# Kernel optimization log

Measured on AMD Instinct MI355X. Metric: run time of the kernel, lower is better.

## Reference

```python
import jax, jax.numpy as jnp
import numpy as np

B, N_PER, P_PER = 64, 64, 2016   # graphs, nodes/graph, pairs/graph (C(64,2))
IN_DIM, HID, OUT = 64, 128, 10
EDGE_P = 0.125


def _build_graph_structures():
    """Integer preprocessing replicating build_2sets_from_embeddings's
    combinatorics (pairs, iso_type source, triangle-based 2-set edges)."""
    rng = np.random.default_rng(0)
    n, b = N_PER, B
    A = rng.random((b, n, n)) < EDGE_P
    A = np.triu(A, 1)
    A = A | A.transpose(0, 2, 1)                      # symmetric, no self loops
    gs, us, vs = np.nonzero(A)                        # directed edges, both dirs
    edge_index = np.stack([gs * n + us, gs * n + vs]).astype(np.int64)
    batch = np.repeat(np.arange(b), n).astype(np.int64)
    iu, iv = np.triu_indices(n, 1)                    # local pair (u<v) lists
    pidx = np.full((n, n), -1, np.int64)
    pidx[iu, iv] = np.arange(P_PER)
    pidx[iv, iu] = np.arange(P_PER)                   # symmetric lookup = sorted()
    pair_u = (np.arange(b)[:, None] * n + iu[None, :]).ravel().astype(np.int64)
    pair_v = (np.arange(b)[:, None] * n + iv[None, :]).ravel().astype(np.int64)
    iso_type = A[:, iu, iv].astype(np.float32).ravel()[:, None]  # [B*P_PER,1]
    # 2-set edges: pair (u,v) -> sorted(v,w) and sorted(u,w) for every common
    # neighbor w of u and v (matches _build_2set_edges exactly)
    common = A[:, iu, :] & A[:, iv, :]                # (B, P_PER, n)
    g2, ps, ws = np.nonzero(common)
    u, v = iu[ps], iv[ps]
    d1 = pidx[v, ws]
    d2 = pidx[u, ws]
    src = np.concatenate([g2 * P_PER + ps, g2 * P_PER + ps])
    dst = np.concatenate([g2 * P_PER + d1, g2 * P_PER + d2])
    two_edges = np.stack([src, dst]).astype(np.int64)
    two_batch = np.repeat(np.arange(b), P_PER).astype(np.int64)
    return edge_index, batch, pair_u, pair_v, iso_type, two_edges, two_batch


def setup_inputs() -> dict:
    ei, batch, pu, pv, iso, te, tb = _build_graph_structures()
    key = jax.random.key(0)
    ks = jax.random.split(key, 16)
    w = lambda k, i, o: jax.random.normal(k, (i, o), jnp.float32) / np.float32(np.sqrt(i))
    two_in = 2 * HID + 1
    return {
        "x": jax.random.normal(ks[0], (B * N_PER, IN_DIM), jnp.float32),
        "g1_W1_0": w(ks[1], IN_DIM, HID), "g1_W2_0": w(ks[2], IN_DIM, HID),
        "g1_W1_1": w(ks[3], HID, HID),    "g1_W2_1": w(ks[4], HID, HID),
        "g1_W1_2": w(ks[5], HID, HID),    "g1_W2_2": w(ks[6], HID, HID),
        "k_W1_0": w(ks[7], two_in, HID),  "k_W2_0": w(ks[8], two_in, HID),
        "k_W1_1": w(ks[9], HID, HID),     "k_W2_1": w(ks[10], HID, HID),
        "c_W0": w(ks[11], 2 * HID, HID),  "c_b0": jnp.zeros((HID,), jnp.float32),
        "c_W1": w(ks[12], HID, OUT),      "c_b1": jnp.zeros((OUT,), jnp.float32),
        "iso_type": jnp.asarray(iso),
        "edge_index": jnp.asarray(ei), "batch": jnp.asarray(batch),
        "pair_u": jnp.asarray(pu), "pair_v": jnp.asarray(pv),
        "two_edges": jnp.asarray(te), "two_batch": jnp.asarray(tb),
    }


def _mp_layer(h, ei, W1, W2):
    # relu( h @ W1 + scatter_add_{dst}( h[src] @ W2 ) )  -- OneGNNLayer / KSetLayer
    msg = h[ei[0]] @ W2
    agg = jax.ops.segment_sum(msg, ei[1], num_segments=h.shape[0])
    return jax.nn.relu(h @ W1 + agg)


def reference(x, g1_W1_0, g1_W2_0, g1_W1_1, g1_W2_1, g1_W1_2, g1_W2_2,
              k_W1_0, k_W2_0, k_W1_1, k_W2_1,
              c_W0, c_b0, c_W1, c_b1,
              iso_type, edge_index, batch, pair_u, pair_v, two_edges, two_batch):
    h = _mp_layer(x, edge_index, g1_W1_0, g1_W2_0)
    h = _mp_layer(h, edge_index, g1_W1_1, g1_W2_1)
    h = _mp_layer(h, edge_index, g1_W1_2, g1_W2_2)
    graph_emb_1 = jax.ops.segment_sum(h, batch, num_segments=B)
    # 2-set features: [h_u, h_v, iso_type]  -> [P, 2H+1]
    two_x = jnp.concatenate([h[pair_u], h[pair_v], iso_type], axis=1)
    h2 = _mp_layer(two_x, two_edges, k_W1_0, k_W2_0)
    h2 = _mp_layer(h2, two_edges, k_W1_1, k_W2_1)
    graph_emb_2 = jax.ops.segment_sum(h2, two_batch, num_segments=B)
    combined = jnp.concatenate([graph_emb_1, graph_emb_2], axis=1)
    hc = jax.nn.relu(combined @ c_W0 + c_b0)   # Dropout(p=0.5) inactive in eval
    return hc @ c_W1 + c_b1
```

## Files before the change

kernel.cpp:

```cpp
#include <hip/hip_runtime.h>
#include <hip/hip_bf16.h>


typedef short s16x8 __attribute__((ext_vector_type(8)));
typedef float f32x4 __attribute__((ext_vector_type(4)));

__device__ __forceinline__ unsigned short f2bf(float f) {
  union { float f; unsigned u; } x; x.f = f;
  unsigned r = (x.u + 0x7fffu + ((x.u >> 16) & 1u)) >> 16;
  return (unsigned short)r;
}
__device__ __forceinline__ float bf2f(unsigned short h) {
  union { unsigned u; float f; } x; x.u = ((unsigned)h) << 16;
  return x.f;
}
__device__ __forceinline__ float4 ldbf4(const unsigned short* p) {
  ushort4 q = *(const ushort4*)p;
  return make_float4(bf2f(q.x), bf2f(q.y), bf2f(q.z), bf2f(q.w));
}
__device__ __forceinline__ void stbf4(unsigned short* p, float4 v) {
  ushort4 q;
  q.x = f2bf(v.x); q.y = f2bf(v.y); q.z = f2bf(v.z); q.w = f2bf(v.w);
  *(ushort4*)p = q;
}
__device__ __forceinline__ float4 ld4(const float* p) { return *(const float4*)p; }

template<int KCS, int ASTR>
__device__ __forceinline__ void mfma_dual_lds(
    const unsigned short* A, const unsigned short* Wfrag,
    f32x4 (&accA)[8], f32x4 (&accB)[8])
{
  const int lane = threadIdx.x & 63;
  const int wv = threadIdx.x >> 6;
  const int row = wv * 16 + (lane & 15);
  const int k0 = (lane >> 4) << 3;
  const unsigned short* ap = A + row * ASTR + k0;
  const unsigned short* wp = Wfrag + (size_t)lane * 8;
#pragma unroll
  for (int i = 0; i < 8; ++i) { accA[i] = (f32x4)0.f; accB[i] = (f32x4)0.f; }
#pragma unroll
  for (int kc = 0; kc < KCS; ++kc) {
    s16x8 af = *(const s16x8*)(ap + kc * 32);
#pragma unroll
    for (int nt = 0; nt < 8; ++nt) {
      s16x8 b0 = *(const s16x8*)(wp + ((size_t)((nt)*KCS + kc) << 9));
      s16x8 b1 = *(const s16x8*)(wp + ((size_t)((8 + nt) * KCS + kc) << 9));
      accA[nt] = __builtin_amdgcn_mfma_f32_16x16x32_bf16(af, b0, accA[nt], 0, 0, 0);
      accB[nt] = __builtin_amdgcn_mfma_f32_16x16x32_bf16(af, b1, accB[nt], 0, 0, 0);
    }
  }
}

template<int KCS, int ASTR>
__device__ __forceinline__ void mfma_dual_lds8(
    const unsigned short* A, const unsigned short* Wfrag,
    f32x4 (&accA)[4], f32x4 (&accB)[4])
{
  const int lane = threadIdx.x & 63;
  const int wv8 = threadIdx.x >> 6;
  const int rw = wv8 & 3, ch = wv8 >> 2;
  const int row = rw * 16 + (lane & 15);
  const int k0 = (lane >> 4) << 3;
  const unsigned short* ap = A + row * ASTR + k0;
  const unsigned short* wp = Wfrag + (size_t)lane * 8;
#pragma unroll
  for (int i = 0; i < 4; ++i) { accA[i] = (f32x4)0.f; accB[i] = (f32x4)0.f; }
  __builtin_amdgcn_s_setprio(1);
#pragma unroll
  for (int kc = 0; kc < KCS; ++kc) {
    s16x8 af = *(const s16x8*)(ap + kc * 32);
#pragma unroll
    for (int n4 = 0; n4 < 4; ++n4) {
      int nt = ch * 4 + n4;
      s16x8 b0 = *(const s16x8*)(wp + ((size_t)(nt * KCS + kc) << 9));
      s16x8 b1 = *(const s16x8*)(wp + ((size_t)((8 + nt) * KCS + kc) << 9));
      accA[n4] = __builtin_amdgcn_mfma_f32_16x16x32_bf16(af, b0, accA[n4], 0, 0, 0);
      accB[n4] = __builtin_amdgcn_mfma_f32_16x16x32_bf16(af, b1, accB[n4], 0, 0, 0);
    }
  }
  __builtin_amdgcn_s_setprio(0);
}

__device__ __forceinline__ void epi_lds8(const f32x4 (&accA)[4], const f32x4 (&accB)[4],
    unsigned short (*preS)[136], unsigned short (*msgS)[136])
{
  const int lane = threadIdx.x & 63;
  const int wv8 = threadIdx.x >> 6;
  const int rw = wv8 & 3, ch = wv8 >> 2;
  const int col = lane & 15;
  const int r0 = rw * 16 + ((lane >> 4) << 2);
  __syncthreads();
#pragma unroll
  for (int n4 = 0; n4 < 4; ++n4) {
    int nt = ch * 4 + n4;
#pragma unroll
    for (int r = 0; r < 4; ++r) {
      preS[r0 + r][nt * 16 + col] = f2bf(accA[n4][r]);
      msgS[r0 + r][nt * 16 + col] = f2bf(accB[n4][r]);
    }
  }
  __syncthreads();
}

__device__ __forceinline__ void epi_global(const f32x4 (&accA)[8], const f32x4 (&accB)[8],
    unsigned short (*sOut)[136], unsigned short* Ca, unsigned short* Cb, long tile)
{
  const int tid = threadIdx.x;
  const int lane = tid & 63;
  const int wv = tid >> 6;
  const int col = lane & 15;
  const int r0 = wv * 16 + ((lane >> 4) << 2);
  const long rowBase = tile * 64;
#pragma unroll
  for (int sel = 0; sel < 2; ++sel) {
    __syncthreads();
#pragma unroll
    for (int nt = 0; nt < 8; ++nt) {
#pragma unroll
      for (int r = 0; r < 4; ++r)
        sOut[r0 + r][nt * 16 + col] = f2bf(sel ? accB[nt][r] : accA[nt][r]);
    }
    __syncthreads();
    unsigned short* C = sel ? Cb : Ca;
#pragma unroll
    for (int i = 0; i < 4; ++i) {
      int fi = tid + i * 256;
      int row = fi >> 4;
      int c8 = fi & 15;
      *(uint4*)(C + (rowBase + row) * 128 + c8 * 8) = *(uint4*)&sOut[row][c8 * 8];
    }
  }
}

struct NArgs {
  const float* x;
  const int* ei;
  const int* gstart;
  const unsigned short *Wf0, *Wf1, *Wf2;
  unsigned short* Hn;
  float* ge1;
  int E1;
};

__global__ __launch_bounds__(512) void node_stage(NArgs a)
{
  __shared__ __align__(16) unsigned short hS[64][136];
  __shared__ __align__(16) unsigned short preS[64][136];
  __shared__ __align__(16) unsigned short msgS[64][136];
  __shared__ int ldeg[64], lcur[64], loff[65];
  __shared__ unsigned short ledge[1024];
  __shared__ float sge[128];

  const int b = blockIdx.x;
  const int t = threadIdx.x;
  const int base = b * 64;

  const int es = a.gstart[b], ee = a.gstart[b + 1];
  if (t < 64) ldeg[t] = 0;
  if (t < 128) sge[t] = 0.f;
  __syncthreads();
  for (int i = es + t; i < ee; i += 512)
    atomicAdd(&ldeg[a.ei[a.E1 + i] - base], 1);
  __syncthreads();
  if (t < 64) {
    int v = ldeg[t], s = v;
#pragma unroll
    for (int d = 1; d < 64; d <<= 1) {
      int o = __shfl_up(s, d, 64);
      if (t >= d) s += o;
    }
    loff[t] = s - v;
    lcur[t] = s - v;
    if (t == 63) loff[64] = s;
  }
  unsigned short* xs = &preS[0][0];
  for (int i = t; i < 64 * 64; i += 512) {
    int r = i >> 6, c = i & 63;
    xs[r * 72 + c] = f2bf(a.x[(size_t)(base + r) * 64 + c]);
  }
  __syncthreads();
  for (int i = es + t; i < ee; i += 512) {
    int s = a.ei[i] - base, d = a.ei[a.E1 + i] - base;
    int pos = atomicAdd(&lcur[d], 1);
    ledge[pos] = (unsigned short)s;
  }
  __syncthreads();

  f32x4 accA[4], accB[4];
  const int grp = t >> 5, f = (t & 31) * 4;

  mfma_dual_lds8<2, 72>(xs, a.Wf0, accA, accB);
  epi_lds8(accA, accB, preS, msgS);
  for (int r = grp; r < 64; r += 16) {
    float4 acc = ldbf4(&preS[r][f]);
    int j1 = loff[r + 1];
    for (int j = loff[r]; j < j1; ++j) {
      float4 m = ldbf4(&msgS[ledge[j]][f]);
      acc.x += m.x; acc.y += m.y; acc.z += m.z; acc.w += m.w;
    }
    stbf4(&hS[r][f], make_float4(fmaxf(acc.x, 0.f), fmaxf(acc.y, 0.f),
                                 fmaxf(acc.z, 0.f), fmaxf(acc.w, 0.f)));
  }
  __syncthreads();

  mfma_dual_lds8<4, 136>(&hS[0][0], a.Wf1, accA, accB);
  epi_lds8(accA, accB, preS, msgS);
  for (int r = grp; r < 64; r += 16) {
    float4 acc = ldbf4(&preS[r][f]);
    int j1 = loff[r + 1];
    for (int j = loff[r]; j < j1; ++j) {
      float4 m = ldbf4(&msgS[ledge[j]][f]);
      acc.x += m.x; acc.y += m.y; acc.z += m.z; acc.w += m.w;
    }
    stbf4(&hS[r][f], make_float4(fmaxf(acc.x, 0.f), fmaxf(acc.y, 0.f),
                                 fmaxf(acc.z, 0.f), fmaxf(acc.w, 0.f)));
  }
  __syncthreads();

  mfma_dual_lds8<4, 136>(&hS[0][0], a.Wf2, accA, accB);
  epi_lds8(accA, accB, preS, msgS);
  {
    float4 g = make_float4(0.f, 0.f, 0.f, 0.f);
    for (int r = grp; r < 64; r += 16) {
      float4 acc = ldbf4(&preS[r][f]);
      int j1 = loff[r + 1];
      for (int j = loff[r]; j < j1; ++j) {
        float4 m = ldbf4(&msgS[ledge[j]][f]);
        acc.x += m.x; acc.y += m.y; acc.z += m.z; acc.w += m.w;
      }
      float4 o = make_float4(fmaxf(acc.x, 0.f), fmaxf(acc.y, 0.f),
                             fmaxf(acc.z, 0.f), fmaxf(acc.w, 0.f));
      stbf4(&hS[r][f], o);
      g.x += o.x; g.y += o.y; g.z += o.z; g.w += o.w;
    }
    atomicAdd(&sge[f + 0], g.x);
    atomicAdd(&sge[f + 1], g.y);
    atomicAdd(&sge[f + 2], g.z);
    atomicAdd(&sge[f + 3], g.w);
  }
  __syncthreads();
  if (t < 128) a.ge1[b * 128 + t] = sge[t];
  for (int i = t; i < 1024; i += 512) {
    int row = i >> 4, c8 = i & 15;
    *(uint4*)(a.Hn + (size_t)(base + row) * 128 + c8 * 8) = *(uint4*)&hS[row][c8 * 8];
  }
}

__global__ __launch_bounds__(256) void hv_gemm(
    const unsigned short* __restrict__ Hn,
    const unsigned short* __restrict__ Wf3, const unsigned short* __restrict__ Wf4,
    unsigned short* __restrict__ HU1, unsigned short* __restrict__ HU2,
    unsigned short* __restrict__ HV1, unsigned short* __restrict__ HV2)
{
  __shared__ __align__(16) unsigned short hS[64][136];
  const int g = blockIdx.x >> 1;
  const int sel = blockIdx.x & 1;
  const int tid = threadIdx.x;
  const unsigned short* src = Hn + (size_t)g * 64 * 128;
#pragma unroll
  for (int i = 0; i < 4; ++i) {
    int fi = tid + i * 256;
    int row = fi >> 4, c8 = fi & 15;
    *(uint4*)&hS[row][c8 * 8] = *(const uint4*)(src + row * 128 + c8 * 8);
  }
  __syncthreads();
  f32x4 accA[8], accB[8];
  mfma_dual_lds<4, 136>(&hS[0][0], sel ? Wf4 : Wf3, accA, accB);
  epi_global(accA, accB, hS, sel ? HV1 : HU1, sel ? HV2 : HU2, g);
}

struct PrepArgs {
  const float* wa[6];
  const float* wb[6];
  unsigned short* Wf[6];
  float* ge2;
  const int* te; int E2;
  int* degP;
  const int* ei; int E1;
  int* gstart;
  int nCnt;
};

__global__ void prep(PrepArgs p)
{
  int bb = blockIdx.x, t = threadIdx.x;
  if (bb < 88) {
    int gid = bb * 256 + t;
    if (gid < 22528) {
      int pi, local, kcs, kclog;
      if (gid < 2048) { pi = 0; local = gid; kcs = 2; kclog = 1; }
      else { int r = gid - 2048; pi = 1 + (r >> 12); local = r & 4095; kcs = 4; kclog = 2; }
      int lane = local & 63;
      int t1 = local >> 6;
      int kc = t1 & (kcs - 1);
      int t2 = t1 >> kclog;
      int nt = t2 & 7;
      int wsel = t2 >> 3;
      const float* W = wsel ? p.wb[pi] : p.wa[pi];
      int k0 = kc * 32 + ((lane >> 4) << 3);
      int n = nt * 16 + (lane & 15);
      unsigned short tmp[8];
#pragma unroll
      for (int j = 0; j < 8; ++j) tmp[j] = f2bf(W[(size_t)(k0 + j) * 128 + n]);
      *(uint4*)(p.Wf[pi] + (size_t)local * 8) = *(uint4*)tmp;
    }
  } else if (bb < 120) {
    int i = (bb - 88) * 256 + t;
    if (i < 8192) p.ge2[i] = 0.f;
  } else if (bb < 120 + p.nCnt) {
    int e = (bb - 120) * 256 + t;
    if (e < p.E2) atomicAdd(&p.degP[p.te[p.E2 + e]], 1);
  } else {
    int e = (bb - 120 - p.nCnt) * 256 + t;
    if (e <= p.E1) {
      int ge = (e < p.E1) ? (p.ei[e] >> 6) : 64;
      int gp = (e > 0) ? (p.ei[e - 1] >> 6) : -1;
      for (int g = gp + 1; g <= ge; ++g) p.gstart[g] = e;
    }
  }
}

__global__ __launch_bounds__(256) void scan_reduce(const int* __restrict__ deg,
                                                   int* __restrict__ bsum, int n)
{
  __shared__ int s[256];
  int b = blockIdx.x, t = threadIdx.x;
  int base = b * 1024;
  int v = 0;
#pragma unroll
  for (int i = 0; i < 4; ++i) {
    int idx = base + t + i * 256;
    if (idx < n) v += deg[idx];
  }
  s[t] = v;
  __syncthreads();
  for (int d = 128; d > 0; d >>= 1) {
    if (t < d) s[t] += s[t + d];
    __syncthreads();
  }
  if (t == 0) bsum[b] = s[0];
}

__global__ __launch_bounds__(1024) void scan_partials(int* __restrict__ bsum, int nb)
{
  __shared__ int s[1024];
  int t = threadIdx.x;
  s[t] = (t < nb) ? bsum[t] : 0;
  __syncthreads();
  for (int d = 1; d < 1024; d <<= 1) {
    int v = (t >= d) ? s[t - d] : 0;
    __syncthreads();
    s[t] += v;
    __syncthreads();
  }
  if (t < nb) bsum[t] = (t == 0) ? 0 : s[t - 1];
  if (t == 1023) bsum[nb] = s[1023];
}

__global__ __launch_bounds__(256) void scan_final(const int* __restrict__ deg,
                                                  const int* __restrict__ bsum,
                                                  int* __restrict__ off,
                                                  int* __restrict__ cur, int n, int nb)
{
  __shared__ int s[256];
  int b = blockIdx.x, t = threadIdx.x;
  int base = b * 1024 + t * 4;
  int v0 = 0, v1 = 0, v2 = 0, v3 = 0;
  if (base + 0 < n) v0 = deg[base + 0];
  if (base + 1 < n) v1 = deg[base + 1];
  if (base + 2 < n) v2 = deg[base + 2];
  if (base + 3 < n) v3 = deg[base + 3];
  s[t] = v0 + v1 + v2 + v3;
  __syncthreads();
  for (int d = 1; d < 256; d <<= 1) {
    int v = (t >= d) ? s[t - d] : 0;
    __syncthreads();
    s[t] += v;
    __syncthreads();
  }
  int run = bsum[b] + ((t == 0) ? 0 : s[t - 1]);
  if (base + 0 < n) { off[base + 0] = run; cur[base + 0] = run; run += v0; }
  if (base + 1 < n) { off[base + 1] = run; cur[base + 1] = run; run += v1; }
  if (base + 2 < n) { off[base + 2] = run; cur[base + 2] = run; run += v2; }
  if (base + 3 < n) { off[base + 3] = run; cur[base + 3] = run; run += v3; }
  if (b == 0 && t == 0) off[n] = bsum[nb];
}

__global__ void csr_fill_pair(const int* __restrict__ te, int E2,
                              const int* __restrict__ pu, const int* __restrict__ pv,
                              const float* __restrict__ iso,
                              int* __restrict__ curP, int4* __restrict__ recP)
{
  int e = blockIdx.x * 256 + threadIdx.x;
  if (e >= E2) return;
  int s = te[e], d = te[E2 + e];
  int pos = atomicAdd(&curP[d], 1);
  recP[pos] = make_int4(pu[s], pv[s], __float_as_int(iso[s]), s);
}

__global__ __launch_bounds__(256) void gather_two0_t(
    const unsigned short* __restrict__ HU1, const unsigned short* __restrict__ HV1,
    const unsigned short* __restrict__ HU2, const unsigned short* __restrict__ HV2,
    const float* __restrict__ iso,
    const float* __restrict__ w1iso, const float* __restrict__ w2iso,
    const int* __restrict__ pu, const int* __restrict__ pv,
    const int* __restrict__ off, const int4* __restrict__ rec,
    unsigned short* __restrict__ out)
{
  __shared__ int offS[65];
  __shared__ int puS[64], pvS[64];
  __shared__ float isoS[64];
  __shared__ __align__(16) int4 recS[512];

  const int tid = threadIdx.x;
  int tile = (int)blockIdx.x;
  const int nT = (int)gridDim.x;
  if ((nT & 7) == 0)
    tile = (tile & 7) * (nT >> 3) + (tile >> 3);
  const int p0 = tile * 64;

  if (tid < 65) offS[tid] = off[p0 + tid];
  if (tid < 64) { puS[tid] = pu[p0 + tid]; pvS[tid] = pv[p0 + tid]; isoS[tid] = iso[p0 + tid]; }
  __syncthreads();
  const int e0 = offS[0];
  const int ecnt = offS[64] - e0;
  const bool useS = (ecnt <= 512);
  if (useS)
    for (int j = tid; j < ecnt; j += 256) recS[j] = rec[e0 + j];
  __syncthreads();

  const int grp = tid >> 5;
  const int f = (tid & 31) * 4;
  const float4 wi1 = ld4(w1iso + f);
  const float4 wi2 = ld4(w2iso + f);
  for (int pi = grp; pi < 64; pi += 8) {
    float4 a = ldbf4(HU1 + (size_t)puS[pi] * 128 + f);
    float4 b = ldbf4(HV1 + (size_t)pvS[pi] * 128 + f);
    float is0 = isoS[pi];
    float4 acc;
    acc.x = a.x + b.x + is0 * wi1.x;
    acc.y = a.y + b.y + is0 * wi1.y;
    acc.z = a.z + b.z + is0 * wi1.z;
    acc.w = a.w + b.w + is0 * wi1.w;
    int j = offS[pi], e1 = offS[pi + 1];
    for (; j + 1 < e1; j += 2) {
      int4 r0 = useS ? recS[j - e0] : rec[j];
      int4 r1 = useS ? recS[j + 1 - e0] : rec[j + 1];
      float4 mu0 = ldbf4(HU2 + (size_t)r0.x * 128 + f);
      float4 mv0 = ldbf4(HV2 + (size_t)r0.y * 128 + f);
      float4 mu1 = ldbf4(HU2 + (size_t)r1.x * 128 + f);
      float4 mv1 = ldbf4(HV2 + (size_t)r1.y * 128 + f);
      float i0 = __int_as_float(r0.z), i1 = __int_as_float(r1.z);
      acc.x += mu0.x + mv0.x + i0 * wi2.x + mu1.x + mv1.x + i1 * wi2.x;
      acc.y += mu0.y + mv0.y + i0 * wi2.y + mu1.y + mv1.y + i1 * wi2.y;
      acc.z += mu0.z + mv0.z + i0 * wi2.z + mu1.z + mv1.z + i1 * wi2.z;
      acc.w += mu0.w + mv0.w + i0 * wi2.w + mu1.w + mv1.w + i1 * wi2.w;
    }
    if (j < e1) {
      int4 r0 = useS ? recS[j - e0] : rec[j];
      float4 mu0 = ldbf4(HU2 + (size_t)r0.x * 128 + f);
      float4 mv0 = ldbf4(HV2 + (size_t)r0.y * 128 + f);
      float i0 = __int_as_float(r0.z);
      acc.x += mu0.x + mv0.x + i0 * wi2.x;
      acc.y += mu0.y + mv0.y + i0 * wi2.y;
      acc.z += mu0.z + mv0.z + i0 * wi2.z;
      acc.w += mu0.w + mv0.w + i0 * wi2.w;
    }
    stbf4(out + (size_t)(p0 + pi) * 128 + f,
          make_float4(fmaxf(acc.x, 0.f), fmaxf(acc.y, 0.f),
                      fmaxf(acc.z, 0.f), fmaxf(acc.w, 0.f)));
  }
}

__global__ __launch_bounds__(256) void pair_l1_fused(
    const unsigned short* __restrict__ H2,
    const unsigned short* __restrict__ Wfrag,
    const int* __restrict__ off, const int4* __restrict__ rec,
    float* __restrict__ ge2, int ppg)
{
  __shared__ __align__(16) unsigned short aggS[64][136];
  __shared__ int offS[65];
  __shared__ int recwS[768];
  __shared__ float sge[2][128];

  const int tid = threadIdx.x;
  int tile = (int)blockIdx.x;
  const int nT = (int)gridDim.x;
  if ((nT & 7) == 0)
    tile = (tile & 7) * (nT >> 3) + (tile >> 3);
  const int r0 = tile * 64;

  if (tid < 65) offS[tid] = off[r0 + tid];
  if (tid < 128) { sge[0][tid] = 0.f; sge[1][tid] = 0.f; }

  const int lane = tid & 63;
  const int wv = tid >> 6;
  const int arow = wv * 16 + (lane & 15);
  const int k0 = (lane >> 4) << 3;
  const unsigned short* hrow = H2 + (size_t)(r0 + arow) * 128 + k0;
  s16x8 ah[4];
#pragma unroll
  for (int kc = 0; kc < 4; ++kc) ah[kc] = *(const s16x8*)(hrow + kc * 32);

  __syncthreads();
  const int e0 = offS[0];
  const int ecnt = offS[64] - e0;
  const bool useS = (ecnt <= 768);
  if (useS)
    for (int j = tid; j < ecnt; j += 256) recwS[j] = rec[e0 + j].w;
  __syncthreads();

  {
    const int grp = tid >> 5, f = (tid & 31) * 4;
    for (int i = grp; i < 64; i += 8) {
      float4 acc = make_float4(0.f, 0.f, 0.f, 0.f);
      int j = offS[i], e1 = offS[i + 1];
      for (; j + 1 < e1; j += 2) {
        int s0 = useS ? recwS[j - e0] : rec[j].w;
        int s1 = useS ? recwS[j + 1 - e0] : rec[j + 1].w;
        float4 m0 = ldbf4(H2 + (size_t)s0 * 128 + f);
        float4 m1 = ldbf4(H2 + (size_t)s1 * 128 + f);
        acc.x += m0.x + m1.x; acc.y += m0.y + m1.y;
        acc.z += m0.z + m1.z; acc.w += m0.w + m1.w;
      }
      if (j < e1) {
        int s0 = useS ? recwS[j - e0] : rec[j].w;
        float4 m0 = ldbf4(H2 + (size_t)s0 * 128 + f);
        acc.x += m0.x; acc.y += m0.y; acc.z += m0.z; acc.w += m0.w;
      }
      stbf4(&aggS[i][f], acc);
    }
  }
  __syncthreads();

  const unsigned short* gp = &aggS[0][0] + arow * 136 + k0;
  const unsigned short* wp = Wfrag + (size_t)lane * 8;
  f32x4 acc[8];
#pragma unroll
  for (int nt = 0; nt < 8; ++nt) acc[nt] = (f32x4)0.f;
  __builtin_amdgcn_s_setprio(1);
#pragma unroll
  for (int kc = 0; kc < 4; ++kc) {
    s16x8 ag = *(const s16x8*)(gp + kc * 32);
#pragma unroll
    for (int nt = 0; nt < 8; ++nt) {
      s16x8 b0 = *(const s16x8*)(wp + ((size_t)(nt * 4 + kc) << 9));
      s16x8 b1 = *(const s16x8*)(wp + ((size_t)((8 + nt) * 4 + kc) << 9));
      acc[nt] = __builtin_amdgcn_mfma_f32_16x16x32_bf16(ah[kc], b0, acc[nt], 0, 0, 0);
      acc[nt] = __builtin_amdgcn_mfma_f32_16x16x32_bf16(ag, b1, acc[nt], 0, 0, 0);
    }
  }
  __builtin_amdgcn_s_setprio(0);

  const int half = wv >> 1;
  const int col0 = lane & 15;
#pragma unroll
  for (int nt = 0; nt < 8; ++nt) {
    float s = fmaxf(acc[nt][0], 0.f) + fmaxf(acc[nt][1], 0.f)
            + fmaxf(acc[nt][2], 0.f) + fmaxf(acc[nt][3], 0.f);
    atomicAdd(&sge[half][nt * 16 + col0], s);
  }
  __syncthreads();
  const int gLo = r0 / ppg;
  const int gHi = (r0 + 32) / ppg;
  if (tid < 128) atomicAdd(&ge2[gLo * 128 + tid], sge[0][tid]);
  else           atomicAdd(&ge2[gHi * 128 + (tid - 128)], sge[1][tid - 128]);
}

__global__ void classifier(const float* __restrict__ ge1, const float* __restrict__ ge2,
                           const float* __restrict__ W0, const float* __restrict__ b0,
                           const float* __restrict__ W1, const float* __restrict__ b1,
                           float* __restrict__ out)
{
  __shared__ float comb[256];
  __shared__ float hc[128];
  int g = blockIdx.x, t = threadIdx.x;
  comb[t]       = ge1[g * 128 + t];
  comb[t + 128] = ge2[g * 128 + t];
  __syncthreads();
  float s = b0[t];
  for (int k = 0; k < 256; ++k) s += comb[k] * W0[k * 128 + t];
  hc[t] = fmaxf(s, 0.f);
  __syncthreads();
  if (t < 10) {
    float s2 = b1[t];
    for (int k = 0; k < 128; ++k) s2 += hc[k] * W1[k * 10 + t];
    out[g * 10 + t] = s2;
  }
}

extern "C" void kernel_launch(void* const* d_in, const int* in_sizes, int n_in,
                              void* d_out, int out_size, void* d_ws, size_t ws_size,
                              hipStream_t stream)
{
  (void)n_in; (void)out_size; (void)ws_size;
  const float* x       = (const float*)d_in[0];
  const float* g1_W1_0 = (const float*)d_in[1];
  const float* g1_W2_0 = (const float*)d_in[2];
  const float* g1_W1_1 = (const float*)d_in[3];
  const float* g1_W2_1 = (const float*)d_in[4];
  const float* g1_W1_2 = (const float*)d_in[5];
  const float* g1_W2_2 = (const float*)d_in[6];
  const float* k_W1_0  = (const float*)d_in[7];
  const float* k_W2_0  = (const float*)d_in[8];
  const float* k_W1_1  = (const float*)d_in[9];
  const float* k_W2_1  = (const float*)d_in[10];
  const float* c_W0    = (const float*)d_in[11];
  const float* c_b0    = (const float*)d_in[12];
  const float* c_W1    = (const float*)d_in[13];
  const float* c_b1    = (const float*)d_in[14];
  const float* iso     = (const float*)d_in[15];
  const int*   ei      = (const int*)d_in[16];
  const int*   pu      = (const int*)d_in[18];
  const int*   pv      = (const int*)d_in[19];
  const int*   te      = (const int*)d_in[20];

  const int N  = in_sizes[0] / 64;
  const int E1 = in_sizes[16] / 2;
  const int P  = in_sizes[18];
  const int E2 = in_sizes[20] / 2;
  const int B  = 64;
  const int ppg = P / B;

  const size_t NH = (size_t)N * 128;
  const size_t PH = (size_t)P * 128;

  float* ge1 = (float*)d_ws;
  float* ge2 = ge1 + 8192;
  unsigned short* HU1 = (unsigned short*)(ge2 + 8192);
  unsigned short* HV1 = HU1 + NH;
  unsigned short* HU2 = HV1 + NH;
  unsigned short* HV2 = HU2 + NH;
  unsigned short* H2   = HV2 + NH;
  unsigned short* Hn   = H2 + PH;
  unsigned short* Wf0  = Hn + NH;
  unsigned short* Wf1  = Wf0 + 16384;
  unsigned short* Wf2  = Wf1 + 32768;
  unsigned short* Wf3  = Wf2 + 32768;
  unsigned short* Wf4  = Wf3 + 32768;
  unsigned short* Wf5  = Wf4 + 32768;

  size_t ipOff = ((size_t)((char*)(Wf5 + 32768) - (char*)d_ws) + 15) & ~(size_t)15;
  int4* recP   = (int4*)((char*)d_ws + ipOff);
  int* degP    = (int*)(recP + E2);
  int* offP    = degP + P;
  int* curP    = offP + P + 1;
  int* bsumP   = curP + P;
  int* gstartN = bsumP + 128;

  const int nbP  = (P + 1023) / 1024;
  const int nCnt = (E2 + 255) / 256;
  const int nBnd = (E1 + 256) / 256;

  hipMemsetAsync(degP, 0, (size_t)P * 4, stream);

  PrepArgs pa;
  pa.wa[0] = g1_W1_0;           pa.wb[0] = g1_W2_0;
  pa.wa[1] = g1_W1_1;           pa.wb[1] = g1_W2_1;
  pa.wa[2] = g1_W1_2;           pa.wb[2] = g1_W2_2;
  pa.wa[3] = k_W1_0;            pa.wb[3] = k_W2_0;
  pa.wa[4] = k_W1_0 + 128*128;  pa.wb[4] = k_W2_0 + 128*128;
  pa.wa[5] = k_W1_1;            pa.wb[5] = k_W2_1;
  pa.Wf[0] = Wf0; pa.Wf[1] = Wf1; pa.Wf[2] = Wf2;
  pa.Wf[3] = Wf3; pa.Wf[4] = Wf4; pa.Wf[5] = Wf5;
  pa.ge2 = ge2; pa.te = te; pa.E2 = E2; pa.degP = degP;
  pa.ei = ei; pa.E1 = E1; pa.gstart = gstartN; pa.nCnt = nCnt;
  prep<<<120 + nCnt + nBnd, 256, 0, stream>>>(pa);

  scan_reduce<<<nbP, 256, 0, stream>>>(degP, bsumP, P);
  scan_partials<<<1, 1024, 0, stream>>>(bsumP, nbP);
  scan_final<<<nbP, 256, 0, stream>>>(degP, bsumP, offP, curP, P, nbP);
  csr_fill_pair<<<nCnt, 256, 0, stream>>>(te, E2, pu, pv, iso, curP, recP);

  NArgs na;
  na.x = x; na.ei = ei; na.gstart = gstartN; na.E1 = E1;
  na.Wf0 = Wf0; na.Wf1 = Wf1; na.Wf2 = Wf2;
  na.Hn = Hn; na.ge1 = ge1;
  node_stage<<<B, 512, 0, stream>>>(na);

  hv_gemm<<<2 * B, 256, 0, stream>>>(Hn, Wf3, Wf4, HU1, HU2, HV1, HV2);

  gather_two0_t<<<P / 64, 256, 0, stream>>>(HU1, HV1, HU2, HV2, iso,
                                            k_W1_0 + 256 * 128, k_W2_0 + 256 * 128,
                                            pu, pv, offP, recP, H2);

  pair_l1_fused<<<P / 64, 256, 0, stream>>>(H2, Wf5, offP, recP, ge2, ppg);

  classifier<<<B, 128, 0, stream>>>(ge1, ge2, c_W0, c_b0, c_W1, c_b1, (float*)d_out);
}
```

Baseline: 304.7 us.

## Switch pair aggregation to edge-parallel LDS atomics and widen node stage to 1024 threads

```diff
diff --git a/kernel.cpp b/kernel.cpp
--- a/kernel.cpp
+++ b/kernel.cpp
@@ -52,51 +52,51 @@
 }
 
 template<int KCS, int ASTR>
-__device__ __forceinline__ void mfma_dual_lds8(
+__device__ __forceinline__ void mfma_dual_lds16(
     const unsigned short* A, const unsigned short* Wfrag,
-    f32x4 (&accA)[4], f32x4 (&accB)[4])
+    f32x4 (&accA)[2], f32x4 (&accB)[2])
 {
   const int lane = threadIdx.x & 63;
-  const int wv8 = threadIdx.x >> 6;
-  const int rw = wv8 & 3, ch = wv8 >> 2;
+  const int w16 = threadIdx.x >> 6;
+  const int rw = w16 & 3, ch = w16 >> 2;
   const int row = rw * 16 + (lane & 15);
   const int k0 = (lane >> 4) << 3;
   const unsigned short* ap = A + row * ASTR + k0;
   const unsigned short* wp = Wfrag + (size_t)lane * 8;
-#pragma unroll
-  for (int i = 0; i < 4; ++i) { accA[i] = (f32x4)0.f; accB[i] = (f32x4)0.f; }
+  accA[0] = (f32x4)0.f; accA[1] = (f32x4)0.f;
+  accB[0] = (f32x4)0.f; accB[1] = (f32x4)0.f;
   __builtin_amdgcn_s_setprio(1);
 #pragma unroll
   for (int kc = 0; kc < KCS; ++kc) {
     s16x8 af = *(const s16x8*)(ap + kc * 32);
 #pragma unroll
-    for (int n4 = 0; n4 < 4; ++n4) {
-      int nt = ch * 4 + n4;
+    for (int n2 = 0; n2 < 2; ++n2) {
+      int nt = ch * 2 + n2;
       s16x8 b0 = *(const s16x8*)(wp + ((size_t)(nt * KCS + kc) << 9));
       s16x8 b1 = *(const s16x8*)(wp + ((size_t)((8 + nt) * KCS + kc) << 9));
-      accA[n4] = __builtin_amdgcn_mfma_f32_16x16x32_bf16(af, b0, accA[n4], 0, 0, 0);
-      accB[n4] = __builtin_amdgcn_mfma_f32_16x16x32_bf16(af, b1, accB[n4], 0, 0, 0);
+      accA[n2] = __builtin_amdgcn_mfma_f32_16x16x32_bf16(af, b0, accA[n2], 0, 0, 0);
+      accB[n2] = __builtin_amdgcn_mfma_f32_16x16x32_bf16(af, b1, accB[n2], 0, 0, 0);
     }
   }
   __builtin_amdgcn_s_setprio(0);
 }
 
-__device__ __forceinline__ void epi_lds8(const f32x4 (&accA)[4], const f32x4 (&accB)[4],
+__device__ __forceinline__ void epi_lds16(const f32x4 (&accA)[2], const f32x4 (&accB)[2],
     unsigned short (*preS)[136], unsigned short (*msgS)[136])
 {
   const int lane = threadIdx.x & 63;
-  const int wv8 = threadIdx.x >> 6;
-  const int rw = wv8 & 3, ch = wv8 >> 2;
+  const int w16 = threadIdx.x >> 6;
+  const int rw = w16 & 3, ch = w16 >> 2;
   const int col = lane & 15;
   const int r0 = rw * 16 + ((lane >> 4) << 2);
   __syncthreads();
 #pragma unroll
-  for (int n4 = 0; n4 < 4; ++n4) {
-    int nt = ch * 4 + n4;
+  for (int n2 = 0; n2 < 2; ++n2) {
+    int nt = ch * 2 + n2;
 #pragma unroll
     for (int r = 0; r < 4; ++r) {
-      preS[r0 + r][nt * 16 + col] = f2bf(accA[n4][r]);
-      msgS[r0 + r][nt * 16 + col] = f2bf(accB[n4][r]);
+      preS[r0 + r][nt * 16 + col] = f2bf(accA[n2][r]);
+      msgS[r0 + r][nt * 16 + col] = f2bf(accB[n2][r]);
     }
   }
   __syncthreads();
@@ -142,7 +142,7 @@
   int E1;
 };
 
-__global__ __launch_bounds__(512) void node_stage(NArgs a)
+__global__ __launch_bounds__(1024) void node_stage(NArgs a)
 {
   __shared__ __align__(16) unsigned short hS[64][136];
   __shared__ __align__(16) unsigned short preS[64][136];
@@ -159,7 +159,7 @@
   if (t < 64) ldeg[t] = 0;
   if (t < 128) sge[t] = 0.f;
   __syncthreads();
-  for (int i = es + t; i < ee; i += 512)
+  for (int i = es + t; i < ee; i += 1024)
     atomicAdd(&ldeg[a.ei[a.E1 + i] - base], 1);
   __syncthreads();
   if (t < 64) {
@@ -174,24 +174,24 @@
     if (t == 63) loff[64] = s;
   }
   unsigned short* xs = &preS[0][0];
-  for (int i = t; i < 64 * 64; i += 512) {
+  for (int i = t; i < 64 * 64; i += 1024) {
     int r = i >> 6, c = i & 63;
     xs[r * 72 + c] = f2bf(a.x[(size_t)(base + r) * 64 + c]);
   }
   __syncthreads();
-  for (int i = es + t; i < ee; i += 512) {
+  for (int i = es + t; i < ee; i += 1024) {
     int s = a.ei[i] - base, d = a.ei[a.E1 + i] - base;
     int pos = atomicAdd(&lcur[d], 1);
     ledge[pos] = (unsigned short)s;
   }
   __syncthreads();
 
-  f32x4 accA[4], accB[4];
+  f32x4 accA[2], accB[2];
   const int grp = t >> 5, f = (t & 31) * 4;
 
-  mfma_dual_lds8<2, 72>(xs, a.Wf0, accA, accB);
-  epi_lds8(accA, accB, preS, msgS);
-  for (int r = grp; r < 64; r += 16) {
+  mfma_dual_lds16<2, 72>(xs, a.Wf0, accA, accB);
+  epi_lds16(accA, accB, preS, msgS);
+  for (int r = grp; r < 64; r += 32) {
     float4 acc = ldbf4(&preS[r][f]);
     int j1 = loff[r + 1];
     for (int j = loff[r]; j < j1; ++j) {
@@ -203,9 +203,9 @@
   }
   __syncthreads();
 
-  mfma_dual_lds8<4, 136>(&hS[0][0], a.Wf1, accA, accB);
-  epi_lds8(accA, accB, preS, msgS);
-  for (int r = grp; r < 64; r += 16) {
+  mfma_dual_lds16<4, 136>(&hS[0][0], a.Wf1, accA, accB);
+  epi_lds16(accA, accB, preS, msgS);
+  for (int r = grp; r < 64; r += 32) {
     float4 acc = ldbf4(&preS[r][f]);
     int j1 = loff[r + 1];
     for (int j = loff[r]; j < j1; ++j) {
@@ -217,11 +217,11 @@
   }
   __syncthreads();
 
-  mfma_dual_lds8<4, 136>(&hS[0][0], a.Wf2, accA, accB);
-  epi_lds8(accA, accB, preS, msgS);
+  mfma_dual_lds16<4, 136>(&hS[0][0], a.Wf2, accA, accB);
+  epi_lds16(accA, accB, preS, msgS);
   {
     float4 g = make_float4(0.f, 0.f, 0.f, 0.f);
-    for (int r = grp; r < 64; r += 16) {
+    for (int r = grp; r < 64; r += 32) {
       float4 acc = ldbf4(&preS[r][f]);
       int j1 = loff[r + 1];
       for (int j = loff[r]; j < j1; ++j) {
@@ -240,8 +240,8 @@
   }
   __syncthreads();
   if (t < 128) a.ge1[b * 128 + t] = sge[t];
-  for (int i = t; i < 1024; i += 512) {
-    int row = i >> 4, c8 = i & 15;
+  {
+    int row = t >> 4, c8 = t & 15;
     *(uint4*)(a.Hn + (size_t)(base + row) * 128 + c8 * 8) = *(uint4*)&hS[row][c8 * 8];
   }
 }
@@ -398,7 +398,7 @@
   recP[pos] = make_int4(pu[s], pv[s], __float_as_int(iso[s]), s);
 }
 
-__global__ __launch_bounds__(256) void gather_two0_t(
+__global__ __launch_bounds__(256) void gather_two0_ep(
     const unsigned short* __restrict__ HU1, const unsigned short* __restrict__ HV1,
     const unsigned short* __restrict__ HU2, const unsigned short* __restrict__ HV2,
     const float* __restrict__ iso,
@@ -407,10 +407,12 @@
     const int* __restrict__ off, const int4* __restrict__ rec,
     unsigned short* __restrict__ out)
 {
+  __shared__ float aggF[64][132];
   __shared__ int offS[65];
   __shared__ int puS[64], pvS[64];
   __shared__ float isoS[64];
   __shared__ __align__(16) int4 recS[512];
+  __shared__ unsigned short dstS[512];
 
   const int tid = threadIdx.x;
   int tile = (int)blockIdx.x;
@@ -421,66 +423,72 @@
 
   if (tid < 65) offS[tid] = off[p0 + tid];
   if (tid < 64) { puS[tid] = pu[p0 + tid]; pvS[tid] = pv[p0 + tid]; isoS[tid] = iso[p0 + tid]; }
+  {
+    float4 z = make_float4(0.f, 0.f, 0.f, 0.f);
+    float4* af = (float4*)&aggF[0][0];
+    for (int i = tid; i < 64 * 132 / 4; i += 256) af[i] = z;
+  }
   __syncthreads();
   const int e0 = offS[0];
   const int ecnt = offS[64] - e0;
   const bool useS = (ecnt <= 512);
-  if (useS)
+  if (useS) {
     for (int j = tid; j < ecnt; j += 256) recS[j] = rec[e0 + j];
+    if (tid < 64) {
+      int j1 = offS[tid + 1] - e0;
+      for (int j = offS[tid] - e0; j < j1; ++j) dstS[j] = (unsigned short)tid;
+    }
+  }
   __syncthreads();
 
   const int grp = tid >> 5;
   const int f = (tid & 31) * 4;
+  const float4 wi2 = ld4(w2iso + f);
+  for (int j = grp; j < ecnt; j += 8) {
+    int4 r; int d;
+    if (useS) { r = recS[j]; d = dstS[j]; }
+    else {
+      r = rec[e0 + j];
+      int lo = 0, hi = 64;
+      while (hi - lo > 1) { int mid = (lo + hi) >> 1; if (offS[mid] <= e0 + j) lo = mid; else hi = mid; }
+      d = lo;
+    }
+    float4 mu = ldbf4(HU2 + (size_t)r.x * 128 + f);
+    float4 mv = ldbf4(HV2 + (size_t)r.y * 128 + f);
+    float i0 = __int_as_float(r.z);
+    atomicAdd(&aggF[d][f + 0], mu.x + mv.x + i0 * wi2.x);
+    atomicAdd(&aggF[d][f + 1], mu.y + mv.y + i0 * wi2.y);
+    atomicAdd(&aggF[d][f + 2], mu.z + mv.z + i0 * wi2.z);
+    atomicAdd(&aggF[d][f + 3], mu.w + mv.w + i0 * wi2.w);
+  }
+  __syncthreads();
+
   const float4 wi1 = ld4(w1iso + f);
-  const float4 wi2 = ld4(w2iso + f);
   for (int pi = grp; pi < 64; pi += 8) {
     float4 a = ldbf4(HU1 + (size_t)puS[pi] * 128 + f);
     float4 b = ldbf4(HV1 + (size_t)pvS[pi] * 128 + f);
     float is0 = isoS[pi];
     float4 acc;
-    acc.x = a.x + b.x + is0 * wi1.x;
-    acc.y = a.y + b.y + is0 * wi1.y;
-    acc.z = a.z + b.z + is0 * wi1.z;
-    acc.w = a.w + b.w + is0 * wi1.w;
-    int j = offS[pi], e1 = offS[pi + 1];
-    for (; j + 1 < e1; j += 2) {
-      int4 r0 = useS ? recS[j - e0] : rec[j];
-      int4 r1 = useS ? recS[j + 1 - e0] : rec[j + 1];
-      float4 mu0 = ldbf4(HU2 + (size_t)r0.x * 128 + f);
-      float4 mv0 = ldbf4(HV2 + (size_t)r0.y * 128 + f);
-      float4 mu1 = ldbf4(HU2 + (size_t)r1.x * 128 + f);
-      float4 mv1 = ldbf4(HV2 + (size_t)r1.y * 128 + f);
-      float i0 = __int_as_float(r0.z), i1 = __int_as_float(r1.z);
-      acc.x += mu0.x + mv0.x + i0 * wi2.x + mu1.x + mv1.x + i1 * wi2.x;
-      acc.y += mu0.y + mv0.y + i0 * wi2.y + mu1.y + mv1.y + i1 * wi2.y;
-      acc.z += mu0.z + mv0.z + i0 * wi2.z + mu1.z + mv1.z + i1 * wi2.z;
-      acc.w += mu0.w + mv0.w + i0 * wi2.w + mu1.w + mv1.w + i1 * wi2.w;
-    }
-    if (j < e1) {
-      int4 r0 = useS ? recS[j - e0] : rec[j];
-      float4 mu0 = ldbf4(HU2 + (size_t)r0.x * 128 + f);
-      float4 mv0 = ldbf4(HV2 + (size_t)r0.y * 128 + f);
-      float i0 = __int_as_float(r0.z);
-      acc.x += mu0.x + mv0.x + i0 * wi2.x;
-      acc.y += mu0.y + mv0.y + i0 * wi2.y;
-      acc.z += mu0.z + mv0.z + i0 * wi2.z;
-      acc.w += mu0.w + mv0.w + i0 * wi2.w;
-    }
+    acc.x = a.x + b.x + is0 * wi1.x + aggF[pi][f + 0];
+    acc.y = a.y + b.y + is0 * wi1.y + aggF[pi][f + 1];
+    acc.z = a.z + b.z + is0 * wi1.z + aggF[pi][f + 2];
+    acc.w = a.w + b.w + is0 * wi1.w + aggF[pi][f + 3];
     stbf4(out + (size_t)(p0 + pi) * 128 + f,
           make_float4(fmaxf(acc.x, 0.f), fmaxf(acc.y, 0.f),
                       fmaxf(acc.z, 0.f), fmaxf(acc.w, 0.f)));
   }
 }
 
-__global__ __launch_bounds__(256) void pair_l1_fused(
+__global__ __launch_bounds__(256) void pair_l1_ep(
     const unsigned short* __restrict__ H2,
     const unsigned short* __restrict__ Wfrag,
     const int* __restrict__ off, const int4* __restrict__ rec,
     float* __restrict__ ge2, int ppg)
 {
-  __shared__ __align__(16) unsigned short aggS[64][136];
+  __shared__ float aggF[64][132];
   __shared__ int offS[65];
-  __shared__ int recwS[768];
+  __shared__ int srcS[512];
+  __shared__ unsigned short dstS[512];
   __shared__ float sge[2][128];
 
   const int tid = threadIdx.x;
@@ -492,6 +500,11 @@
 
   if (tid < 65) offS[tid] = off[r0 + tid];
   if (tid < 128) { sge[0][tid] = 0.f; sge[1][tid] = 0.f; }
+  {
+    float4 z = make_float4(0.f, 0.f, 0.f, 0.f);
+    float4* af = (float4*)&aggF[0][0];
+    for (int i = tid; i < 64 * 132 / 4; i += 256) af[i] = z;
+  }
 
   const int lane = tid & 63;
   const int wv = tid >> 6;
@@ -505,35 +518,35 @@
   __syncthreads();
   const int e0 = offS[0];
   const int ecnt = offS[64] - e0;
-  const bool useS = (ecnt <= 768);
-  if (useS)
-    for (int j = tid; j < ecnt; j += 256) recwS[j] = rec[e0 + j].w;
-  __syncthreads();
-
-  {
-    const int grp = tid >> 5, f = (tid & 31) * 4;
-    for (int i = grp; i < 64; i += 8) {
-      float4 acc = make_float4(0.f, 0.f, 0.f, 0.f);
-      int j = offS[i], e1 = offS[i + 1];
-      for (; j + 1 < e1; j += 2) {
-        int s0 = useS ? recwS[j - e0] : rec[j].w;
-        int s1 = useS ? recwS[j + 1 - e0] : rec[j + 1].w;
-        float4 m0 = ldbf4(H2 + (size_t)s0 * 128 + f);
-        float4 m1 = ldbf4(H2 + (size_t)s1 * 128 + f);
-        acc.x += m0.x + m1.x; acc.y += m0.y + m1.y;
-        acc.z += m0.z + m1.z; acc.w += m0.w + m1.w;
-      }
-      if (j < e1) {
-        int s0 = useS ? recwS[j - e0] : rec[j].w;
-        float4 m0 = ldbf4(H2 + (size_t)s0 * 128 + f);
-        acc.x += m0.x; acc.y += m0.y; acc.z += m0.z; acc.w += m0.w;
-      }
-      stbf4(&aggS[i][f], acc);
-    }
-  }
-  __syncthreads();
-
-  const unsigned short* gp = &aggS[0][0] + arow * 136 + k0;
+  const bool useS = (ecnt <= 512);
+  if (useS) {
+    for (int j = tid; j < ecnt; j += 256) srcS[j] = rec[e0 + j].w;
+    if (tid < 64) {
+      int j1 = offS[tid + 1] - e0;
+      for (int j = offS[tid] - e0; j < j1; ++j) dstS[j] = (unsigned short)tid;
+    }
+  }
+  __syncthreads();
+
+  const int grp = tid >> 5;
+  const int f = (tid & 31) * 4;
+  for (int j = grp; j < ecnt; j += 8) {
+    int s, d;
+    if (useS) { s = srcS[j]; d = dstS[j]; }
+    else {
+      s = rec[e0 + j].w;
+      int lo = 0, hi = 64;
+      while (hi - lo > 1) { int mid = (lo + hi) >> 1; if (offS[mid] <= e0 + j) lo = mid; else hi = mid; }
+      d = lo;
+    }
+    float4 m = ldbf4(H2 + (size_t)s * 128 + f);
+    atomicAdd(&aggF[d][f + 0], m.x);
+    atomicAdd(&aggF[d][f + 1], m.y);
+    atomicAdd(&aggF[d][f + 2], m.z);
+    atomicAdd(&aggF[d][f + 3], m.w);
+  }
+  __syncthreads();
+
   const unsigned short* wp = Wfrag + (size_t)lane * 8;
   f32x4 acc[8];
 #pragma unroll
@@ -541,7 +554,13 @@
   __builtin_amdgcn_s_setprio(1);
 #pragma unroll
   for (int kc = 0; kc < 4; ++kc) {
-    s16x8 ag = *(const s16x8*)(gp + kc * 32);
+    float4 lo = *(const float4*)&aggF[arow][kc * 32 + k0];
+    float4 hi = *(const float4*)&aggF[arow][kc * 32 + k0 + 4];
+    s16x8 ag;
+    ag[0] = (short)f2bf(lo.x); ag[1] = (short)f2bf(lo.y);
+    ag[2] = (short)f2bf(lo.z); ag[3] = (short)f2bf(lo.w);
+    ag[4] = (short)f2bf(hi.x); ag[5] = (short)f2bf(hi.y);
+    ag[6] = (short)f2bf(hi.z); ag[7] = (short)f2bf(hi.w);
 #pragma unroll
     for (int nt = 0; nt < 8; ++nt) {
       s16x8 b0 = *(const s16x8*)(wp + ((size_t)(nt * 4 + kc) << 9));
@@ -676,15 +695,15 @@
   na.x = x; na.ei = ei; na.gstart = gstartN; na.E1 = E1;
   na.Wf0 = Wf0; na.Wf1 = Wf1; na.Wf2 = Wf2;
   na.Hn = Hn; na.ge1 = ge1;
-  node_stage<<<B, 512, 0, stream>>>(na);
+  node_stage<<<B, 1024, 0, stream>>>(na);
 
   hv_gemm<<<2 * B, 256, 0, stream>>>(Hn, Wf3, Wf4, HU1, HU2, HV1, HV2);
 
-  gather_two0_t<<<P / 64, 256, 0, stream>>>(HU1, HV1, HU2, HV2, iso,
-                                            k_W1_0 + 256 * 128, k_W2_0 + 256 * 128,
-                                            pu, pv, offP, recP, H2);
-
-  pair_l1_fused<<<P / 64, 256, 0, stream>>>(H2, Wf5, offP, recP, ge2, ppg);
+  gather_two0_ep<<<P / 64, 256, 0, stream>>>(HU1, HV1, HU2, HV2, iso,
+                                             k_W1_0 + 256 * 128, k_W2_0 + 256 * 128,
+                                             pu, pv, offP, recP, H2);
+
+  pair_l1_ep<<<P / 64, 256, 0, stream>>>(H2, Wf5, offP, recP, ge2, ppg);
 
   classifier<<<B, 128, 0, stream>>>(ge1, ge2, c_W0, c_b0, c_W1, c_b1, (float*)d_out);
 }
```

New measurement: 667.0 us. 119% more time.

## Widen node stage to 1024 threads and replace ge2 atomics with per-tile partials

Applied to the files above, without the earlier changes.

```diff
diff --git a/kernel.cpp b/kernel.cpp
--- a/kernel.cpp
+++ b/kernel.cpp
@@ -52,51 +52,51 @@
 }
 
 template<int KCS, int ASTR>
-__device__ __forceinline__ void mfma_dual_lds8(
+__device__ __forceinline__ void mfma_dual_lds16(
     const unsigned short* A, const unsigned short* Wfrag,
-    f32x4 (&accA)[4], f32x4 (&accB)[4])
+    f32x4 (&accA)[2], f32x4 (&accB)[2])
 {
   const int lane = threadIdx.x & 63;
-  const int wv8 = threadIdx.x >> 6;
-  const int rw = wv8 & 3, ch = wv8 >> 2;
+  const int w16 = threadIdx.x >> 6;
+  const int rw = w16 & 3, ch = w16 >> 2;
   const int row = rw * 16 + (lane & 15);
   const int k0 = (lane >> 4) << 3;
   const unsigned short* ap = A + row * ASTR + k0;
   const unsigned short* wp = Wfrag + (size_t)lane * 8;
-#pragma unroll
-  for (int i = 0; i < 4; ++i) { accA[i] = (f32x4)0.f; accB[i] = (f32x4)0.f; }
+  accA[0] = (f32x4)0.f; accA[1] = (f32x4)0.f;
+  accB[0] = (f32x4)0.f; accB[1] = (f32x4)0.f;
   __builtin_amdgcn_s_setprio(1);
 #pragma unroll
   for (int kc = 0; kc < KCS; ++kc) {
     s16x8 af = *(const s16x8*)(ap + kc * 32);
 #pragma unroll
-    for (int n4 = 0; n4 < 4; ++n4) {
-      int nt = ch * 4 + n4;
+    for (int n2 = 0; n2 < 2; ++n2) {
+      int nt = ch * 2 + n2;
       s16x8 b0 = *(const s16x8*)(wp + ((size_t)(nt * KCS + kc) << 9));
       s16x8 b1 = *(const s16x8*)(wp + ((size_t)((8 + nt) * KCS + kc) << 9));
-      accA[n4] = __builtin_amdgcn_mfma_f32_16x16x32_bf16(af, b0, accA[n4], 0, 0, 0);
-      accB[n4] = __builtin_amdgcn_mfma_f32_16x16x32_bf16(af, b1, accB[n4], 0, 0, 0);
+      accA[n2] = __builtin_amdgcn_mfma_f32_16x16x32_bf16(af, b0, accA[n2], 0, 0, 0);
+      accB[n2] = __builtin_amdgcn_mfma_f32_16x16x32_bf16(af, b1, accB[n2], 0, 0, 0);
     }
   }
   __builtin_amdgcn_s_setprio(0);
 }
 
-__device__ __forceinline__ void epi_lds8(const f32x4 (&accA)[4], const f32x4 (&accB)[4],
+__device__ __forceinline__ void epi_lds16(const f32x4 (&accA)[2], const f32x4 (&accB)[2],
     unsigned short (*preS)[136], unsigned short (*msgS)[136])
 {
   const int lane = threadIdx.x & 63;
-  const int wv8 = threadIdx.x >> 6;
-  const int rw = wv8 & 3, ch = wv8 >> 2;
+  const int w16 = threadIdx.x >> 6;
+  const int rw = w16 & 3, ch = w16 >> 2;
   const int col = lane & 15;
   const int r0 = rw * 16 + ((lane >> 4) << 2);
   __syncthreads();
 #pragma unroll
-  for (int n4 = 0; n4 < 4; ++n4) {
-    int nt = ch * 4 + n4;
+  for (int n2 = 0; n2 < 2; ++n2) {
+    int nt = ch * 2 + n2;
 #pragma unroll
     for (int r = 0; r < 4; ++r) {
-      preS[r0 + r][nt * 16 + col] = f2bf(accA[n4][r]);
-      msgS[r0 + r][nt * 16 + col] = f2bf(accB[n4][r]);
+      preS[r0 + r][nt * 16 + col] = f2bf(accA[n2][r]);
+      msgS[r0 + r][nt * 16 + col] = f2bf(accB[n2][r]);
     }
   }
   __syncthreads();
@@ -142,7 +142,7 @@
   int E1;
 };
 
-__global__ __launch_bounds__(512) void node_stage(NArgs a)
+__global__ __launch_bounds__(1024) void node_stage(NArgs a)
 {
   __shared__ __align__(16) unsigned short hS[64][136];
   __shared__ __align__(16) unsigned short preS[64][136];
@@ -159,7 +159,7 @@
   if (t < 64) ldeg[t] = 0;
   if (t < 128) sge[t] = 0.f;
   __syncthreads();
-  for (int i = es + t; i < ee; i += 512)
+  for (int i = es + t; i < ee; i += 1024)
     atomicAdd(&ldeg[a.ei[a.E1 + i] - base], 1);
   __syncthreads();
   if (t < 64) {
@@ -174,24 +174,24 @@
     if (t == 63) loff[64] = s;
   }
   unsigned short* xs = &preS[0][0];
-  for (int i = t; i < 64 * 64; i += 512) {
+  for (int i = t; i < 64 * 64; i += 1024) {
     int r = i >> 6, c = i & 63;
     xs[r * 72 + c] = f2bf(a.x[(size_t)(base + r) * 64 + c]);
   }
   __syncthreads();
-  for (int i = es + t; i < ee; i += 512) {
+  for (int i = es + t; i < ee; i += 1024) {
     int s = a.ei[i] - base, d = a.ei[a.E1 + i] - base;
     int pos = atomicAdd(&lcur[d], 1);
     ledge[pos] = (unsigned short)s;
   }
   __syncthreads();
 
-  f32x4 accA[4], accB[4];
+  f32x4 accA[2], accB[2];
   const int grp = t >> 5, f = (t & 31) * 4;
 
-  mfma_dual_lds8<2, 72>(xs, a.Wf0, accA, accB);
-  epi_lds8(accA, accB, preS, msgS);
-  for (int r = grp; r < 64; r += 16) {
+  mfma_dual_lds16<2, 72>(xs, a.Wf0, accA, accB);
+  epi_lds16(accA, accB, preS, msgS);
+  for (int r = grp; r < 64; r += 32) {
     float4 acc = ldbf4(&preS[r][f]);
     int j1 = loff[r + 1];
     for (int j = loff[r]; j < j1; ++j) {
@@ -203,9 +203,9 @@
   }
   __syncthreads();
 
-  mfma_dual_lds8<4, 136>(&hS[0][0], a.Wf1, accA, accB);
-  epi_lds8(accA, accB, preS, msgS);
-  for (int r = grp; r < 64; r += 16) {
+  mfma_dual_lds16<4, 136>(&hS[0][0], a.Wf1, accA, accB);
+  epi_lds16(accA, accB, preS, msgS);
+  for (int r = grp; r < 64; r += 32) {
     float4 acc = ldbf4(&preS[r][f]);
     int j1 = loff[r + 1];
     for (int j = loff[r]; j < j1; ++j) {
@@ -217,11 +217,11 @@
   }
   __syncthreads();
 
-  mfma_dual_lds8<4, 136>(&hS[0][0], a.Wf2, accA, accB);
-  epi_lds8(accA, accB, preS, msgS);
+  mfma_dual_lds16<4, 136>(&hS[0][0], a.Wf2, accA, accB);
+  epi_lds16(accA, accB, preS, msgS);
   {
     float4 g = make_float4(0.f, 0.f, 0.f, 0.f);
-    for (int r = grp; r < 64; r += 16) {
+    for (int r = grp; r < 64; r += 32) {
       float4 acc = ldbf4(&preS[r][f]);
       int j1 = loff[r + 1];
       for (int j = loff[r]; j < j1; ++j) {
@@ -240,8 +240,8 @@
   }
   __syncthreads();
   if (t < 128) a.ge1[b * 128 + t] = sge[t];
-  for (int i = t; i < 1024; i += 512) {
-    int row = i >> 4, c8 = i & 15;
+  {
+    int row = t >> 4, c8 = t & 15;
     *(uint4*)(a.Hn + (size_t)(base + row) * 128 + c8 * 8) = *(uint4*)&hS[row][c8 * 8];
   }
 }
@@ -273,7 +273,6 @@
   const float* wa[6];
   const float* wb[6];
   unsigned short* Wf[6];
-  float* ge2;
   const int* te; int E2;
   int* degP;
   const int* ei; int E1;
@@ -304,14 +303,11 @@
       for (int j = 0; j < 8; ++j) tmp[j] = f2bf(W[(size_t)(k0 + j) * 128 + n]);
       *(uint4*)(p.Wf[pi] + (size_t)local * 8) = *(uint4*)tmp;
     }
-  } else if (bb < 120) {
-    int i = (bb - 88) * 256 + t;
-    if (i < 8192) p.ge2[i] = 0.f;
-  } else if (bb < 120 + p.nCnt) {
-    int e = (bb - 120) * 256 + t;
+  } else if (bb < 88 + p.nCnt) {
+    int e = (bb - 88) * 256 + t;
     if (e < p.E2) atomicAdd(&p.degP[p.te[p.E2 + e]], 1);
   } else {
-    int e = (bb - 120 - p.nCnt) * 256 + t;
+    int e = (bb - 88 - p.nCnt) * 256 + t;
     if (e <= p.E1) {
       int ge = (e < p.E1) ? (p.ei[e] >> 6) : 64;
       int gp = (e > 0) ? (p.ei[e - 1] >> 6) : -1;
@@ -472,16 +468,16 @@
   }
 }
 
-__global__ __launch_bounds__(256) void pair_l1_fused(
+__global__ __launch_bounds__(256) void pair_l1(
     const unsigned short* __restrict__ H2,
     const unsigned short* __restrict__ Wfrag,
     const int* __restrict__ off, const int4* __restrict__ rec,
-    float* __restrict__ ge2, int ppg)
+    float* __restrict__ gep)
 {
   __shared__ __align__(16) unsigned short aggS[64][136];
   __shared__ int offS[65];
   __shared__ int recwS[768];
-  __shared__ float sge[2][128];
+  __shared__ float sge[256];
 
   const int tid = threadIdx.x;
   int tile = (int)blockIdx.x;
@@ -491,7 +487,7 @@
   const int r0 = tile * 64;
 
   if (tid < 65) offS[tid] = off[r0 + tid];
-  if (tid < 128) { sge[0][tid] = 0.f; sge[1][tid] = 0.f; }
+  sge[tid] = 0.f;
 
   const int lane = tid & 63;
   const int wv = tid >> 6;
@@ -558,16 +554,13 @@
   for (int nt = 0; nt < 8; ++nt) {
     float s = fmaxf(acc[nt][0], 0.f) + fmaxf(acc[nt][1], 0.f)
             + fmaxf(acc[nt][2], 0.f) + fmaxf(acc[nt][3], 0.f);
-    atomicAdd(&sge[half][nt * 16 + col0], s);
-  }
-  __syncthreads();
-  const int gLo = r0 / ppg;
-  const int gHi = (r0 + 32) / ppg;
-  if (tid < 128) atomicAdd(&ge2[gLo * 128 + tid], sge[0][tid]);
-  else           atomicAdd(&ge2[gHi * 128 + (tid - 128)], sge[1][tid - 128]);
-}
-
-__global__ void classifier(const float* __restrict__ ge1, const float* __restrict__ ge2,
+    atomicAdd(&sge[half * 128 + nt * 16 + col0], s);
+  }
+  __syncthreads();
+  gep[(size_t)tile * 256 + tid] = sge[tid];
+}
+
+__global__ void classifier(const float* __restrict__ ge1, const float* __restrict__ gep,
                            const float* __restrict__ W0, const float* __restrict__ b0,
                            const float* __restrict__ W1, const float* __restrict__ b1,
                            float* __restrict__ out)
@@ -575,17 +568,20 @@
   __shared__ float comb[256];
   __shared__ float hc[128];
   int g = blockIdx.x, t = threadIdx.x;
-  comb[t]       = ge1[g * 128 + t];
-  comb[t + 128] = ge2[g * 128 + t];
+  comb[t] = ge1[g * 128 + t];
+  float s2 = 0.f;
+  const float* gpr = gep + (size_t)g * 63 * 128 + t;
+  for (int i = 0; i < 63; ++i) s2 += gpr[i * 128];
+  comb[t + 128] = s2;
   __syncthreads();
   float s = b0[t];
   for (int k = 0; k < 256; ++k) s += comb[k] * W0[k * 128 + t];
   hc[t] = fmaxf(s, 0.f);
   __syncthreads();
   if (t < 10) {
-    float s2 = b1[t];
-    for (int k = 0; k < 128; ++k) s2 += hc[k] * W1[k * 10 + t];
-    out[g * 10 + t] = s2;
+    float s2o = b1[t];
+    for (int k = 0; k < 128; ++k) s2o += hc[k] * W1[k * 10 + t];
+    out[g * 10 + t] = s2o;
   }
 }
 
@@ -620,14 +616,14 @@
   const int P  = in_sizes[18];
   const int E2 = in_sizes[20] / 2;
   const int B  = 64;
-  const int ppg = P / B;
+  const int nTiles = P / 64;
 
   const size_t NH = (size_t)N * 128;
   const size_t PH = (size_t)P * 128;
 
   float* ge1 = (float*)d_ws;
-  float* ge2 = ge1 + 8192;
-  unsigned short* HU1 = (unsigned short*)(ge2 + 8192);
+  float* gep = ge1 + 8192;
+  unsigned short* HU1 = (unsigned short*)(gep + (size_t)2 * nTiles * 128);
   unsigned short* HV1 = HU1 + NH;
   unsigned short* HU2 = HV1 + NH;
   unsigned short* HV2 = HU2 + NH;
@@ -663,9 +659,9 @@
   pa.wa[5] = k_W1_1;            pa.wb[5] = k_W2_1;
   pa.Wf[0] = Wf0; pa.Wf[1] = Wf1; pa.Wf[2] = Wf2;
   pa.Wf[3] = Wf3; pa.Wf[4] = Wf4; pa.Wf[5] = Wf5;
-  pa.ge2 = ge2; pa.te = te; pa.E2 = E2; pa.degP = degP;
+  pa.te = te; pa.E2 = E2; pa.degP = degP;
   pa.ei = ei; pa.E1 = E1; pa.gstart = gstartN; pa.nCnt = nCnt;
-  prep<<<120 + nCnt + nBnd, 256, 0, stream>>>(pa);
+  prep<<<88 + nCnt + nBnd, 256, 0, stream>>>(pa);
 
   scan_reduce<<<nbP, 256, 0, stream>>>(degP, bsumP, P);
   scan_partials<<<1, 1024, 0, stream>>>(bsumP, nbP);
@@ -676,15 +672,15 @@
   na.x = x; na.ei = ei; na.gstart = gstartN; na.E1 = E1;
   na.Wf0 = Wf0; na.Wf1 = Wf1; na.Wf2 = Wf2;
   na.Hn = Hn; na.ge1 = ge1;
-  node_stage<<<B, 512, 0, stream>>>(na);
+  node_stage<<<B, 1024, 0, stream>>>(na);
 
   hv_gemm<<<2 * B, 256, 0, stream>>>(Hn, Wf3, Wf4, HU1, HU2, HV1, HV2);
 
-  gather_two0_t<<<P / 64, 256, 0, stream>>>(HU1, HV1, HU2, HV2, iso,
+  gather_two0_t<<<nTiles, 256, 0, stream>>>(HU1, HV1, HU2, HV2, iso,
                                             k_W1_0 + 256 * 128, k_W2_0 + 256 * 128,
                                             pu, pv, offP, recP, H2);
 
-  pair_l1_fused<<<P / 64, 256, 0, stream>>>(H2, Wf5, offP, recP, ge2, ppg);
-
-  classifier<<<B, 128, 0, stream>>>(ge1, ge2, c_W0, c_b0, c_W1, c_b1, (float*)d_out);
-}
+  pair_l1<<<nTiles, 256, 0, stream>>>(H2, Wf5, offP, recP, gep);
+
+  classifier<<<B, 128, 0, stream>>>(ge1, gep, c_W0, c_b0, c_W1, c_b1, (float*)d_out);
+}
```

New measurement: 302.4 us, median of 2. Within noise of the previous version (-0.8%).
